# Kernel optimization log

Hardware: AMD Instinct MI355X
Metric: run time of the kernel (lower is better)

## Reference

```python
import jax, jax.numpy as jnp
import numpy as np

DIM = 64  # matches init kwarg `dim`; temperature = sqrt(DIM)


def setup_inputs() -> dict:
    key = jax.random.key(0)
    kq, kk, kv = jax.random.split(key, 3)
    B, Lq, Lk, d = 16, 4096, 4096, DIM
    q = jax.random.normal(kq, (B, Lq, d), dtype=jnp.float32)
    k = jax.random.normal(kk, (B, Lk, d), dtype=jnp.float32)
    v = jax.random.normal(kv, (B, Lk, d), dtype=jnp.float32)
    return {"q": q, "k": k, "v": v}


def reference(q, k, v):
    # attn = softmax(q @ k^T / sqrt(dim)); dropout is identity in eval mode.
    temperature = jnp.asarray(np.sqrt(DIM), dtype=q.dtype)
    scores = jnp.einsum('bqd,bkd->bqk', q, k) / temperature  # [B, Lq, Lk]
    attn = jax.nn.softmax(scores, axis=-1)
    out = jnp.einsum('bqk,bkd->bqd', attn, v)  # [B, Lq, d]
    return out
```

## Files before the change

kernel.cpp:

```cpp
#include <hip/hip_runtime.h>
#include <stdint.h>
#include <math.h>

typedef __attribute__((ext_vector_type(2)))  float f2;
typedef __attribute__((ext_vector_type(4)))  float f4;
typedef __attribute__((ext_vector_type(16))) float f32x16;
typedef __attribute__((ext_vector_type(8)))  short bf16x8;

#define NB   16
#define LSEQ 4096
#define DH   64
#define QB   128
#define KVB  64
#define NT   (LSEQ / KVB)

__device__ __forceinline__ short f2bf(float f) {
    union { float f; uint32_t u; } v; v.f = f;
    return (short)((v.u + 0x7FFFu + ((v.u >> 16) & 1u)) >> 16);
}

__device__ __forceinline__ uint32_t cvtpk(float lo, float hi) {
    uint32_t r;
    asm("v_cvt_pk_bf16_f32 %0, %1, %2" : "=v"(r) : "v"(lo), "v"(hi));
    return r;
}

__global__ __launch_bounds__(256, 2) void fa_fwd(
    const float* __restrict__ Q, const float* __restrict__ K,
    const float* __restrict__ V, float* __restrict__ O)
{
    __shared__ __align__(16) short k_lds[2][KVB * DH];
    __shared__ __align__(16) short v_lds[2][DH * KVB];

    const int tid  = threadIdx.x;
    const int lane = tid & 63;
    const int w    = tid >> 6;
    const int l31  = lane & 31;
    const int H    = lane >> 5;

    const int bid  = blockIdx.x;
    const int xcd  = bid & 7;
    const int slot = bid >> 3;
    const int b    = xcd * 2 + (slot >> 5);
    const int qt   = slot & 31;
    const int q0   = qt * QB + w * 32;

    const float* Qb = Q + (size_t)b * LSEQ * DH;
    const float* Kb = K + (size_t)b * LSEQ * DH;
    const float* Vb = V + (size_t)b * LSEQ * DH;
    float*       Ob = O + (size_t)b * LSEQ * DH;

    const float QS = 0.125f * 1.44269504088896340736f;

    bf16x8 qf[4];
#pragma unroll
    for (int kb = 0; kb < 4; ++kb) {
        const float* src = Qb + (size_t)(q0 + l31) * DH + 16 * kb + 8 * H;
        f4 a = *(const f4*)src;
        f4 c = *(const f4*)(src + 4);
        bf16x8 f;
        f[0] = f2bf(a[0] * QS); f[1] = f2bf(a[1] * QS);
        f[2] = f2bf(a[2] * QS); f[3] = f2bf(a[3] * QS);
        f[4] = f2bf(c[0] * QS); f[5] = f2bf(c[1] * QS);
        f[6] = f2bf(c[2] * QS); f[7] = f2bf(c[3] * QS);
        qf[kb] = f;
    }

    bf16x8 ones;
#pragma unroll
    for (int i = 0; i < 8; ++i) ones[i] = (short)0x3F80;

    f4 kreg[4];
    f2 vreg[8];

    const int k_kv0 = (tid >> 3);
    const int k_d0  = (tid & 7) * 8;
    const int v_d0  = (tid & 31) * 2;
    const int v_g   = tid >> 5;

#define LOADK(KV0)                                                              \
    {                                                                           \
        _Pragma("unroll")                                                       \
        for (int p = 0; p < 2; ++p) {                                           \
            const float* src = Kb + (size_t)((KV0) + k_kv0 + 32 * p) * DH + k_d0; \
            kreg[2 * p]     = *(const f4*)src;                                  \
            kreg[2 * p + 1] = *(const f4*)(src + 4);                            \
        }                                                                       \
        _Pragma("unroll")                                                       \
        for (int j = 0; j < 8; ++j)                                             \
            vreg[j] = *(const f2*)&Vb[(size_t)((KV0) + 8 * v_g + j) * DH + v_d0]; \
    }

#define WRITEK(BUF)                                                             \
    {                                                                           \
        _Pragma("unroll")                                                       \
        for (int p = 0; p < 2; ++p) {                                           \
            const int kv = k_kv0 + 32 * p;                                      \
            union { bf16x8 v; uint32_t u[4]; } t;                               \
            t.u[0] = cvtpk(kreg[2 * p][0], kreg[2 * p][1]);                     \
            t.u[1] = cvtpk(kreg[2 * p][2], kreg[2 * p][3]);                     \
            t.u[2] = cvtpk(kreg[2 * p + 1][0], kreg[2 * p + 1][1]);             \
            t.u[3] = cvtpk(kreg[2 * p + 1][2], kreg[2 * p + 1][3]);             \
            *(bf16x8*)&k_lds[BUF][kv * DH + (k_d0 ^ ((kv & 7) << 3))] = t.v;    \
        }                                                                       \
        _Pragma("unroll")                                                       \
        for (int c = 0; c < 2; ++c) {                                           \
            const int d = v_d0 + c;                                             \
            union { bf16x8 v; uint32_t u[4]; } t;                               \
            t.u[0] = cvtpk(vreg[0][c], vreg[1][c]);                             \
            t.u[1] = cvtpk(vreg[2][c], vreg[3][c]);                             \
            t.u[2] = cvtpk(vreg[4][c], vreg[5][c]);                             \
            t.u[3] = cvtpk(vreg[6][c], vreg[7][c]);                             \
            *(bf16x8*)&v_lds[BUF][d * KVB + 8 * (v_g ^ (d & 7))] = t.v;         \
        }                                                                       \
    }

#define QKH(BUF, D, ROFF)                                                       \
    {                                                                           \
        _Pragma("unroll")                                                       \
        for (int i = 0; i < 16; ++i) D[i] = 0.f;                                \
        _Pragma("unroll")                                                       \
        for (int kb = 0; kb < 4; ++kb) {                                        \
            const int d0 = 16 * kb + 8 * H;                                     \
            bf16x8 kf = *(const bf16x8*)&k_lds[BUF][(ROFF + l31) * DH + (d0 ^ ((l31 & 7) << 3))]; \
            D = __builtin_amdgcn_mfma_f32_32x32x16_bf16(kf, qf[kb], D, 0, 0, 0); \
        }                                                                       \
    }

#define EXP16(S)                                                                \
    {                                                                           \
        _Pragma("unroll")                                                       \
        for (int i = 0; i < 16; ++i) S[i] = __builtin_amdgcn_exp2f(S[i]);       \
    }

#define MAKE_PA(P, ks2, dst)                                                    \
    {                                                                           \
        uint32_t a1 = cvtpk(P[8*(ks2)+0], P[8*(ks2)+1]);                        \
        uint32_t b1 = cvtpk(P[8*(ks2)+4], P[8*(ks2)+5]);                        \
        uint32_t a2 = cvtpk(P[8*(ks2)+2], P[8*(ks2)+3]);                        \
        uint32_t b2 = cvtpk(P[8*(ks2)+6], P[8*(ks2)+7]);                        \
        asm volatile("v_permlane32_swap_b32 %0, %1" : "+v"(a1), "+v"(b1));      \
        asm volatile("v_permlane32_swap_b32 %0, %1" : "+v"(a2), "+v"(b2));      \
        union { bf16x8 v; uint32_t u[4]; } t;                                   \
        t.u[0] = a1; t.u[1] = a2; t.u[2] = b1; t.u[3] = b2;                     \
        dst = t.v;                                                              \
    }

#define PVKS(BUF, ks, pav)                                                      \
    {                                                                           \
        const int d0g = 2 * (ks) + H;                                           \
        bf16x8 vf0 = *(const bf16x8*)&v_lds[BUF][(l31)      * KVB + 8 * (d0g ^ (l31 & 7))]; \
        bf16x8 vf1 = *(const bf16x8*)&v_lds[BUF][(32 + l31) * KVB + 8 * (d0g ^ (l31 & 7))]; \
        oacc0 = __builtin_amdgcn_mfma_f32_32x32x16_bf16(vf0, pav, oacc0, 0, 0, 0); \
        oacc1 = __builtin_amdgcn_mfma_f32_32x32x16_bf16(vf1, pav, oacc1, 0, 0, 0); \
        lacc  = __builtin_amdgcn_mfma_f32_32x32x16_bf16(ones, pav, lacc, 0, 0, 0); \
    }

#define BODY(IT, DO_LOAD, DO_STAGE)                                             \
    {                                                                           \
        const int cur = (IT) & 1;                                               \
        bf16x8 pa0, pa1, pa2, pa3;                                              \
        EXP16(s0);                                                              \
        MAKE_PA(s0, 0, pa0); MAKE_PA(s0, 1, pa1);                               \
        __builtin_amdgcn_s_setprio(1);                                          \
        PVKS(cur, 0, pa0); PVKS(cur, 1, pa1);                                   \
        __builtin_amdgcn_s_setprio(0);                                          \
        EXP16(s1);                                                              \
        MAKE_PA(s1, 0, pa2); MAKE_PA(s1, 1, pa3);                               \
        __builtin_amdgcn_s_setprio(1);                                          \
        PVKS(cur, 2, pa2); PVKS(cur, 3, pa3);                                   \
        __builtin_amdgcn_s_setprio(0);                                          \
        if (DO_STAGE) {                                                         \
            WRITEK(cur ^ 1);                                                    \
            __syncthreads();                                                    \
            if (DO_LOAD) LOADK(((IT) + 2) * KVB);                               \
            __builtin_amdgcn_s_setprio(1);                                      \
            QKH(cur ^ 1, s0, 0); QKH(cur ^ 1, s1, 32);                          \
            __builtin_amdgcn_s_setprio(0);                                      \
        }                                                                       \
    }

    f32x16 oacc0, oacc1, lacc;
#pragma unroll
    for (int i = 0; i < 16; ++i) { oacc0[i] = 0.f; oacc1[i] = 0.f; lacc[i] = 0.f; }

    LOADK(0);
    WRITEK(0);
    __syncthreads();
    LOADK(KVB);

    f32x16 s0, s1;
    QKH(0, s0, 0);
    QKH(0, s1, 32);

    for (int it = 0; it < NT - 2; ++it) BODY(it, 1, 1);
    BODY(NT - 2, 0, 1);
    BODY(NT - 1, 0, 0);

    const float inv = 1.0f / lacc[0];
    const int q = q0 + l31;
#pragma unroll
    for (int k = 0; k < 4; ++k) {
        f4 o0, o1;
#pragma unroll
        for (int m = 0; m < 4; ++m) { o0[m] = oacc0[4*k+m] * inv; o1[m] = oacc1[4*k+m] * inv; }
        *(f4*)&Ob[(size_t)q * DH +      8 * k + 4 * H] = o0;
        *(f4*)&Ob[(size_t)q * DH + 32 + 8 * k + 4 * H] = o1;
    }
#undef LOADK
#undef WRITEK
#undef QKH
#undef EXP16
#undef MAKE_PA
#undef PVKS
#undef BODY
}

extern "C" void kernel_launch(void* const* d_in, const int* in_sizes, int n_in,
                              void* d_out, int out_size, void* d_ws, size_t ws_size,
                              hipStream_t stream) {
    (void)in_sizes; (void)n_in; (void)d_ws; (void)ws_size; (void)out_size;
    const float* q = (const float*)d_in[0];
    const float* k = (const float*)d_in[1];
    const float* v = (const float*)d_in[2];
    float* o = (float*)d_out;
    hipLaunchKernelGGL(fa_fwd, dim3(NB * 32), dim3(256), 0, stream, q, k, v, o);
}
```

Measured before the change: 104.7 us.

## Split KV sequence across two blocks and combine partial outputs in workspace

Templates the attention kernel on a KV split factor. With enough workspace, each (batch, query-tile) is processed by two blocks that each cover half the keys. Each block writes unnormalized partial outputs and row sums to workspace, and a second kernel adds the two halves and normalizes. This doubles the grid and raises launch bounds to four blocks per SM to improve occupancy and latency hiding. In exchange it adds a large workspace write and read-back, a second launch, and possible register pressure from the tighter launch bound.

```diff
diff --git a/kernel.cpp b/kernel.cpp
--- a/kernel.cpp
+++ b/kernel.cpp
@@ -25,12 +25,16 @@
     return r;
 }
 
-__global__ __launch_bounds__(256, 2) void fa_fwd(
+template<int NSPLIT>
+__global__ __launch_bounds__(256, 4) void fa_fwd(
     const float* __restrict__ Q, const float* __restrict__ K,
-    const float* __restrict__ V, float* __restrict__ O)
+    const float* __restrict__ V, float* __restrict__ O,
+    float* __restrict__ wsO, float* __restrict__ wsL)
 {
     __shared__ __align__(16) short k_lds[2][KVB * DH];
     __shared__ __align__(16) short v_lds[2][DH * KVB];
+
+    const int NTL = NT / NSPLIT;
 
     const int tid  = threadIdx.x;
     const int lane = tid & 63;
@@ -41,9 +45,19 @@
     const int bid  = blockIdx.x;
     const int xcd  = bid & 7;
     const int slot = bid >> 3;
-    const int b    = xcd * 2 + (slot >> 5);
-    const int qt   = slot & 31;
-    const int q0   = qt * QB + w * 32;
+    int b, h, qt;
+    if (NSPLIT == 2) {
+        const int u = slot >> 5;
+        qt = slot & 31;
+        b  = (xcd << 1) | (u >> 1);
+        h  = u & 1;
+    } else {
+        qt = slot & 31;
+        b  = xcd * 2 + (slot >> 5);
+        h  = 0;
+    }
+    const int q0     = qt * QB + w * 32;
+    const int kvbase = h * (LSEQ / NSPLIT);
 
     const float* Qb = Q + (size_t)b * LSEQ * DH;
     const float* Kb = K + (size_t)b * LSEQ * DH;
@@ -173,7 +187,7 @@
         if (DO_STAGE) {                                                         \
             WRITEK(cur ^ 1);                                                    \
             __syncthreads();                                                    \
-            if (DO_LOAD) LOADK(((IT) + 2) * KVB);                               \
+            if (DO_LOAD) LOADK(kvbase + ((IT) + 2) * KVB);                      \
             __builtin_amdgcn_s_setprio(1);                                      \
             QKH(cur ^ 1, s0, 0); QKH(cur ^ 1, s1, 32);                          \
             __builtin_amdgcn_s_setprio(0);                                      \
@@ -184,28 +198,41 @@
 #pragma unroll
     for (int i = 0; i < 16; ++i) { oacc0[i] = 0.f; oacc1[i] = 0.f; lacc[i] = 0.f; }
 
-    LOADK(0);
+    LOADK(kvbase);
     WRITEK(0);
     __syncthreads();
-    LOADK(KVB);
+    LOADK(kvbase + KVB);
 
     f32x16 s0, s1;
     QKH(0, s0, 0);
     QKH(0, s1, 32);
 
-    for (int it = 0; it < NT - 2; ++it) BODY(it, 1, 1);
-    BODY(NT - 2, 0, 1);
-    BODY(NT - 1, 0, 0);
-
-    const float inv = 1.0f / lacc[0];
+    for (int it = 0; it < NTL - 2; ++it) BODY(it, 1, 1);
+    BODY(NTL - 2, 0, 1);
+    BODY(NTL - 1, 0, 0);
+
     const int q = q0 + l31;
-#pragma unroll
-    for (int k = 0; k < 4; ++k) {
-        f4 o0, o1;
-#pragma unroll
-        for (int m = 0; m < 4; ++m) { o0[m] = oacc0[4*k+m] * inv; o1[m] = oacc1[4*k+m] * inv; }
-        *(f4*)&Ob[(size_t)q * DH +      8 * k + 4 * H] = o0;
-        *(f4*)&Ob[(size_t)q * DH + 32 + 8 * k + 4 * H] = o1;
+    if (NSPLIT == 1) {
+        const float inv = 1.0f / lacc[0];
+#pragma unroll
+        for (int k = 0; k < 4; ++k) {
+            f4 o0, o1;
+#pragma unroll
+            for (int m = 0; m < 4; ++m) { o0[m] = oacc0[4*k+m] * inv; o1[m] = oacc1[4*k+m] * inv; }
+            *(f4*)&Ob[(size_t)q * DH +      8 * k + 4 * H] = o0;
+            *(f4*)&Ob[(size_t)q * DH + 32 + 8 * k + 4 * H] = o1;
+        }
+    } else {
+        float* dst = wsO + (size_t)(h * NB + b) * LSEQ * DH;
+#pragma unroll
+        for (int k = 0; k < 4; ++k) {
+            f4 o0, o1;
+#pragma unroll
+            for (int m = 0; m < 4; ++m) { o0[m] = oacc0[4*k+m]; o1[m] = oacc1[4*k+m]; }
+            *(f4*)&dst[(size_t)q * DH +      8 * k + 4 * H] = o0;
+            *(f4*)&dst[(size_t)q * DH + 32 + 8 * k + 4 * H] = o1;
+        }
+        if (H == 0) wsL[(size_t)(h * NB + b) * LSEQ + q] = lacc[0];
     }
 #undef LOADK
 #undef WRITEK
@@ -216,13 +243,41 @@
 #undef BODY
 }
 
+__global__ __launch_bounds__(256) void fa_combine(
+    const float* __restrict__ wsO, const float* __restrict__ wsL,
+    float* __restrict__ O)
+{
+    const size_t HALF = (size_t)NB * LSEQ * DH;
+    const int idx = blockIdx.x * 256 + threadIdx.x;
+    const int row = idx >> 4;
+    f4 a = *(const f4*)&wsO[(size_t)idx * 4];
+    f4 c = *(const f4*)&wsO[HALF + (size_t)idx * 4];
+    const float inv = 1.0f / (wsL[row] + wsL[NB * LSEQ + row]);
+    f4 o;
+#pragma unroll
+    for (int m = 0; m < 4; ++m) o[m] = (a[m] + c[m]) * inv;
+    *(f4*)&O[(size_t)idx * 4] = o;
+}
+
 extern "C" void kernel_launch(void* const* d_in, const int* in_sizes, int n_in,
                               void* d_out, int out_size, void* d_ws, size_t ws_size,
                               hipStream_t stream) {
-    (void)in_sizes; (void)n_in; (void)d_ws; (void)ws_size; (void)out_size;
+    (void)in_sizes; (void)n_in; (void)out_size;
     const float* q = (const float*)d_in[0];
     const float* k = (const float*)d_in[1];
     const float* v = (const float*)d_in[2];
     float* o = (float*)d_out;
-    hipLaunchKernelGGL(fa_fwd, dim3(NB * 32), dim3(256), 0, stream, q, k, v, o);
-}
+
+    const size_t NEED = ((size_t)2 * NB * LSEQ * DH + 2 * NB * LSEQ) * sizeof(float);
+    if (ws_size >= NEED && d_ws != nullptr) {
+        float* wsO = (float*)d_ws;
+        float* wsL = wsO + (size_t)2 * NB * LSEQ * DH;
+        hipLaunchKernelGGL((fa_fwd<2>), dim3(NB * 32 * 2), dim3(256), 0, stream,
+                           q, k, v, o, wsO, wsL);
+        hipLaunchKernelGGL(fa_combine, dim3((NB * LSEQ * DH / 4) / 256), dim3(256), 0, stream,
+                           wsO, wsL, o);
+    } else {
+        hipLaunchKernelGGL((fa_fwd<1>), dim3(NB * 32), dim3(256), 0, stream,
+                           q, k, v, o, nullptr, nullptr);
+    }
+}
```

Result: slower. 279.2 us (+166.6%).

## Double query tile per block and compute row sums on VALU instead of MFMA

Applied to the files above, without the earlier changes.

Grows the query tile to 256 rows with 512 threads per block, so each staged K/V tile is reused by twice as many queries, halving global K/V loads and conversions per query. Replaces the ones-vector MFMA row-sum with a VALU accumulation of the exponentials plus a final lane shuffle, removing a third of the PV-phase MFMAs. The cost is fewer, larger blocks with wider barriers and more register pressure under the new launch bounds.

```diff
diff --git a/kernel.cpp b/kernel.cpp
--- a/kernel.cpp
+++ b/kernel.cpp
@@ -2,7 +2,6 @@
 #include <stdint.h>
 #include <math.h>
 
-typedef __attribute__((ext_vector_type(2)))  float f2;
 typedef __attribute__((ext_vector_type(4)))  float f4;
 typedef __attribute__((ext_vector_type(16))) float f32x16;
 typedef __attribute__((ext_vector_type(8)))  short bf16x8;
@@ -10,7 +9,7 @@
 #define NB   16
 #define LSEQ 4096
 #define DH   64
-#define QB   128
+#define QB   256
 #define KVB  64
 #define NT   (LSEQ / KVB)
 
@@ -25,7 +24,7 @@
     return r;
 }
 
-__global__ __launch_bounds__(256, 2) void fa_fwd(
+__global__ __launch_bounds__(512, 2) void fa_fwd(
     const float* __restrict__ Q, const float* __restrict__ K,
     const float* __restrict__ V, float* __restrict__ O)
 {
@@ -41,8 +40,8 @@
     const int bid  = blockIdx.x;
     const int xcd  = bid & 7;
     const int slot = bid >> 3;
-    const int b    = xcd * 2 + (slot >> 5);
-    const int qt   = slot & 31;
+    const int b    = xcd * 2 + (slot >> 4);
+    const int qt   = slot & 15;
     const int q0   = qt * QB + w * 32;
 
     const float* Qb = Q + (size_t)b * LSEQ * DH;
@@ -66,53 +65,38 @@
         qf[kb] = f;
     }
 
-    bf16x8 ones;
-#pragma unroll
-    for (int i = 0; i < 8; ++i) ones[i] = (short)0x3F80;
-
-    f4 kreg[4];
-    f2 vreg[8];
-
-    const int k_kv0 = (tid >> 3);
-    const int k_d0  = (tid & 7) * 8;
-    const int v_d0  = (tid & 31) * 2;
-    const int v_g   = tid >> 5;
-
-#define LOADK(KV0)                                                              \
-    {                                                                           \
-        _Pragma("unroll")                                                       \
-        for (int p = 0; p < 2; ++p) {                                           \
-            const float* src = Kb + (size_t)((KV0) + k_kv0 + 32 * p) * DH + k_d0; \
-            kreg[2 * p]     = *(const f4*)src;                                  \
-            kreg[2 * p + 1] = *(const f4*)(src + 4);                            \
-        }                                                                       \
+    f4    kreg[2];
+    float vreg[8];
+    const int k_r  = tid >> 3;
+    const int k_d0 = (tid & 7) * 8;
+    const int v_d  = tid & 63;
+    const int v_g  = tid >> 6;
+
+#define LOADT(T)                                                                \
+    {                                                                           \
+        const int kv0 = (T) * KVB;                                              \
+        const float* src = Kb + (size_t)(kv0 + k_r) * DH + k_d0;                \
+        kreg[0] = *(const f4*)src;                                              \
+        kreg[1] = *(const f4*)(src + 4);                                        \
         _Pragma("unroll")                                                       \
         for (int j = 0; j < 8; ++j)                                             \
-            vreg[j] = *(const f2*)&Vb[(size_t)((KV0) + 8 * v_g + j) * DH + v_d0]; \
-    }
-
-#define WRITEK(BUF)                                                             \
-    {                                                                           \
-        _Pragma("unroll")                                                       \
-        for (int p = 0; p < 2; ++p) {                                           \
-            const int kv = k_kv0 + 32 * p;                                      \
-            union { bf16x8 v; uint32_t u[4]; } t;                               \
-            t.u[0] = cvtpk(kreg[2 * p][0], kreg[2 * p][1]);                     \
-            t.u[1] = cvtpk(kreg[2 * p][2], kreg[2 * p][3]);                     \
-            t.u[2] = cvtpk(kreg[2 * p + 1][0], kreg[2 * p + 1][1]);             \
-            t.u[3] = cvtpk(kreg[2 * p + 1][2], kreg[2 * p + 1][3]);             \
-            *(bf16x8*)&k_lds[BUF][kv * DH + (k_d0 ^ ((kv & 7) << 3))] = t.v;    \
-        }                                                                       \
-        _Pragma("unroll")                                                       \
-        for (int c = 0; c < 2; ++c) {                                           \
-            const int d = v_d0 + c;                                             \
-            union { bf16x8 v; uint32_t u[4]; } t;                               \
-            t.u[0] = cvtpk(vreg[0][c], vreg[1][c]);                             \
-            t.u[1] = cvtpk(vreg[2][c], vreg[3][c]);                             \
-            t.u[2] = cvtpk(vreg[4][c], vreg[5][c]);                             \
-            t.u[3] = cvtpk(vreg[6][c], vreg[7][c]);                             \
-            *(bf16x8*)&v_lds[BUF][d * KVB + 8 * (v_g ^ (d & 7))] = t.v;         \
-        }                                                                       \
+            vreg[j] = Vb[(size_t)(kv0 + 8 * v_g + j) * DH + v_d];               \
+    }
+
+#define WRITET(BUF)                                                             \
+    {                                                                           \
+        union { bf16x8 v; uint32_t u[4]; } tk;                                  \
+        tk.u[0] = cvtpk(kreg[0][0], kreg[0][1]);                                \
+        tk.u[1] = cvtpk(kreg[0][2], kreg[0][3]);                                \
+        tk.u[2] = cvtpk(kreg[1][0], kreg[1][1]);                                \
+        tk.u[3] = cvtpk(kreg[1][2], kreg[1][3]);                                \
+        *(bf16x8*)&k_lds[BUF][k_r * DH + (k_d0 ^ ((k_r & 7) << 3))] = tk.v;     \
+        union { bf16x8 v; uint32_t u[4]; } tv;                                  \
+        tv.u[0] = cvtpk(vreg[0], vreg[1]);                                      \
+        tv.u[1] = cvtpk(vreg[2], vreg[3]);                                      \
+        tv.u[2] = cvtpk(vreg[4], vreg[5]);                                      \
+        tv.u[3] = cvtpk(vreg[6], vreg[7]);                                      \
+        *(bf16x8*)&v_lds[BUF][v_d * KVB + 8 * (v_g ^ (v_d & 7))] = tv.v;        \
     }
 
 #define QKH(BUF, D, ROFF)                                                       \
@@ -127,10 +111,17 @@
         }                                                                       \
     }
 
-#define EXP16(S)                                                                \
-    {                                                                           \
-        _Pragma("unroll")                                                       \
-        for (int i = 0; i < 16; ++i) S[i] = __builtin_amdgcn_exp2f(S[i]);       \
+#define EXPSUM(S)                                                               \
+    {                                                                           \
+        float r0 = 0.f, r1 = 0.f, r2 = 0.f, r3 = 0.f;                           \
+        _Pragma("unroll")                                                       \
+        for (int i = 0; i < 4; ++i) {                                           \
+            S[i]      = __builtin_amdgcn_exp2f(S[i]);      r0 += S[i];          \
+            S[i + 4]  = __builtin_amdgcn_exp2f(S[i + 4]);  r1 += S[i + 4];      \
+            S[i + 8]  = __builtin_amdgcn_exp2f(S[i + 8]);  r2 += S[i + 8];      \
+            S[i + 12] = __builtin_amdgcn_exp2f(S[i + 12]); r3 += S[i + 12];     \
+        }                                                                       \
+        l_run += (r0 + r1) + (r2 + r3);                                         \
     }
 
 #define MAKE_PA(P, ks2, dst)                                                    \
@@ -153,41 +144,41 @@
         bf16x8 vf1 = *(const bf16x8*)&v_lds[BUF][(32 + l31) * KVB + 8 * (d0g ^ (l31 & 7))]; \
         oacc0 = __builtin_amdgcn_mfma_f32_32x32x16_bf16(vf0, pav, oacc0, 0, 0, 0); \
         oacc1 = __builtin_amdgcn_mfma_f32_32x32x16_bf16(vf1, pav, oacc1, 0, 0, 0); \
-        lacc  = __builtin_amdgcn_mfma_f32_32x32x16_bf16(ones, pav, lacc, 0, 0, 0); \
     }
 
 #define BODY(IT, DO_LOAD, DO_STAGE)                                             \
     {                                                                           \
         const int cur = (IT) & 1;                                               \
         bf16x8 pa0, pa1, pa2, pa3;                                              \
-        EXP16(s0);                                                              \
+        EXPSUM(s0);                                                             \
         MAKE_PA(s0, 0, pa0); MAKE_PA(s0, 1, pa1);                               \
         __builtin_amdgcn_s_setprio(1);                                          \
         PVKS(cur, 0, pa0); PVKS(cur, 1, pa1);                                   \
         __builtin_amdgcn_s_setprio(0);                                          \
-        EXP16(s1);                                                              \
+        EXPSUM(s1);                                                             \
         MAKE_PA(s1, 0, pa2); MAKE_PA(s1, 1, pa3);                               \
         __builtin_amdgcn_s_setprio(1);                                          \
         PVKS(cur, 2, pa2); PVKS(cur, 3, pa3);                                   \
         __builtin_amdgcn_s_setprio(0);                                          \
         if (DO_STAGE) {                                                         \
-            WRITEK(cur ^ 1);                                                    \
+            WRITET(cur ^ 1);                                                    \
             __syncthreads();                                                    \
-            if (DO_LOAD) LOADK(((IT) + 2) * KVB);                               \
+            if (DO_LOAD) LOADT((IT) + 2);                                       \
             __builtin_amdgcn_s_setprio(1);                                      \
             QKH(cur ^ 1, s0, 0); QKH(cur ^ 1, s1, 32);                          \
             __builtin_amdgcn_s_setprio(0);                                      \
         }                                                                       \
     }
 
-    f32x16 oacc0, oacc1, lacc;
-#pragma unroll
-    for (int i = 0; i < 16; ++i) { oacc0[i] = 0.f; oacc1[i] = 0.f; lacc[i] = 0.f; }
-
-    LOADK(0);
-    WRITEK(0);
+    f32x16 oacc0, oacc1;
+#pragma unroll
+    for (int i = 0; i < 16; ++i) { oacc0[i] = 0.f; oacc1[i] = 0.f; }
+    float l_run = 0.f;
+
+    LOADT(0);
+    WRITET(0);
     __syncthreads();
-    LOADK(KVB);
+    LOADT(1);
 
     f32x16 s0, s1;
     QKH(0, s0, 0);
@@ -197,7 +188,8 @@
     BODY(NT - 2, 0, 1);
     BODY(NT - 1, 0, 0);
 
-    const float inv = 1.0f / lacc[0];
+    l_run += __shfl_xor(l_run, 32);
+    const float inv = 1.0f / l_run;
     const int q = q0 + l31;
 #pragma unroll
     for (int k = 0; k < 4; ++k) {
@@ -207,10 +199,10 @@
         *(f4*)&Ob[(size_t)q * DH +      8 * k + 4 * H] = o0;
         *(f4*)&Ob[(size_t)q * DH + 32 + 8 * k + 4 * H] = o1;
     }
-#undef LOADK
-#undef WRITEK
+#undef LOADT
+#undef WRITET
 #undef QKH
-#undef EXP16
+#undef EXPSUM
 #undef MAKE_PA
 #undef PVKS
 #undef BODY
@@ -224,5 +216,5 @@
     const float* k = (const float*)d_in[1];
     const float* v = (const float*)d_in[2];
     float* o = (float*)d_out;
-    hipLaunchKernelGGL(fa_fwd, dim3(NB * 32), dim3(256), 0, stream, q, k, v, o);
-}
+    hipLaunchKernelGGL(fa_fwd, dim3(NB * (LSEQ / QB)), dim3(512), 0, stream, q, k, v, o);
+}
```

Measured after the change: 87.98 us. 1.19x faster.

## Double per-wave query rows and compute softmax denominator with VALU sums

Applied to the files above, without the earlier changes.

Each wave now handles 64 query rows (two 32-row groups) instead of 32, so the Q tile per block doubles and every K/V fragment read from LDS feeds twice as many MFMAs. The grid halves to 256 blocks and launch bounds drop to one block per SIMD group, which leaves room for the extra accumulator registers. The ones-vector MFMA that computed the row sum is replaced by per-lane exp sums plus a final cross-half shuffle. In exchange the grid is smaller than two waves per CU slot, so occupancy and latency hiding may drop, and register pressure rises.

```diff
diff --git a/kernel.cpp b/kernel.cpp
--- a/kernel.cpp
+++ b/kernel.cpp
@@ -10,7 +10,7 @@
 #define NB   16
 #define LSEQ 4096
 #define DH   64
-#define QB   128
+#define QB   256
 #define KVB  64
 #define NT   (LSEQ / KVB)
 
@@ -25,7 +25,7 @@
     return r;
 }
 
-__global__ __launch_bounds__(256, 2) void fa_fwd(
+__global__ __launch_bounds__(256, 1) void fa_fwd(
     const float* __restrict__ Q, const float* __restrict__ K,
     const float* __restrict__ V, float* __restrict__ O)
 {
@@ -41,9 +41,9 @@
     const int bid  = blockIdx.x;
     const int xcd  = bid & 7;
     const int slot = bid >> 3;
-    const int b    = xcd * 2 + (slot >> 5);
-    const int qt   = slot & 31;
-    const int q0   = qt * QB + w * 32;
+    const int b    = xcd * 2 + (slot >> 4);
+    const int qt   = slot & 15;
+    const int q0   = qt * QB + w * 64;
 
     const float* Qb = Q + (size_t)b * LSEQ * DH;
     const float* Kb = K + (size_t)b * LSEQ * DH;
@@ -52,46 +52,45 @@
 
     const float QS = 0.125f * 1.44269504088896340736f;
 
-    bf16x8 qf[4];
+    bf16x8 qfA[4], qfB[4];
 #pragma unroll
     for (int kb = 0; kb < 4; ++kb) {
-        const float* src = Qb + (size_t)(q0 + l31) * DH + 16 * kb + 8 * H;
-        f4 a = *(const f4*)src;
-        f4 c = *(const f4*)(src + 4);
-        bf16x8 f;
-        f[0] = f2bf(a[0] * QS); f[1] = f2bf(a[1] * QS);
-        f[2] = f2bf(a[2] * QS); f[3] = f2bf(a[3] * QS);
-        f[4] = f2bf(c[0] * QS); f[5] = f2bf(c[1] * QS);
-        f[6] = f2bf(c[2] * QS); f[7] = f2bf(c[3] * QS);
-        qf[kb] = f;
-    }
-
-    bf16x8 ones;
-#pragma unroll
-    for (int i = 0; i < 8; ++i) ones[i] = (short)0x3F80;
+#pragma unroll
+        for (int g = 0; g < 2; ++g) {
+            const float* src = Qb + (size_t)(q0 + 32 * g + l31) * DH + 16 * kb + 8 * H;
+            f4 a = *(const f4*)src;
+            f4 c = *(const f4*)(src + 4);
+            bf16x8 f;
+            f[0] = f2bf(a[0] * QS); f[1] = f2bf(a[1] * QS);
+            f[2] = f2bf(a[2] * QS); f[3] = f2bf(a[3] * QS);
+            f[4] = f2bf(c[0] * QS); f[5] = f2bf(c[1] * QS);
+            f[6] = f2bf(c[2] * QS); f[7] = f2bf(c[3] * QS);
+            if (g == 0) qfA[kb] = f; else qfB[kb] = f;
+        }
+    }
 
     f4 kreg[4];
     f2 vreg[8];
-
     const int k_kv0 = (tid >> 3);
     const int k_d0  = (tid & 7) * 8;
     const int v_d0  = (tid & 31) * 2;
     const int v_g   = tid >> 5;
 
-#define LOADK(KV0)                                                              \
-    {                                                                           \
+#define LOADT(T)                                                                \
+    {                                                                           \
+        const int kv0 = (T) * KVB;                                              \
         _Pragma("unroll")                                                       \
         for (int p = 0; p < 2; ++p) {                                           \
-            const float* src = Kb + (size_t)((KV0) + k_kv0 + 32 * p) * DH + k_d0; \
+            const float* src = Kb + (size_t)(kv0 + k_kv0 + 32 * p) * DH + k_d0; \
             kreg[2 * p]     = *(const f4*)src;                                  \
             kreg[2 * p + 1] = *(const f4*)(src + 4);                            \
         }                                                                       \
         _Pragma("unroll")                                                       \
         for (int j = 0; j < 8; ++j)                                             \
-            vreg[j] = *(const f2*)&Vb[(size_t)((KV0) + 8 * v_g + j) * DH + v_d0]; \
-    }
-
-#define WRITEK(BUF)                                                             \
+            vreg[j] = *(const f2*)&Vb[(size_t)(kv0 + 8 * v_g + j) * DH + v_d0]; \
+    }
+
+#define WRITET(BUF)                                                             \
     {                                                                           \
         _Pragma("unroll")                                                       \
         for (int p = 0; p < 2; ++p) {                                           \
@@ -115,22 +114,33 @@
         }                                                                       \
     }
 
-#define QKH(BUF, D, ROFF)                                                       \
-    {                                                                           \
-        _Pragma("unroll")                                                       \
-        for (int i = 0; i < 16; ++i) D[i] = 0.f;                                \
+#define QK2(BUF)                                                                \
+    {                                                                           \
+        _Pragma("unroll")                                                       \
+        for (int i = 0; i < 16; ++i) { sA0[i] = 0.f; sA1[i] = 0.f; sB0[i] = 0.f; sB1[i] = 0.f; } \
         _Pragma("unroll")                                                       \
         for (int kb = 0; kb < 4; ++kb) {                                        \
             const int d0 = 16 * kb + 8 * H;                                     \
-            bf16x8 kf = *(const bf16x8*)&k_lds[BUF][(ROFF + l31) * DH + (d0 ^ ((l31 & 7) << 3))]; \
-            D = __builtin_amdgcn_mfma_f32_32x32x16_bf16(kf, qf[kb], D, 0, 0, 0); \
-        }                                                                       \
-    }
-
-#define EXP16(S)                                                                \
-    {                                                                           \
-        _Pragma("unroll")                                                       \
-        for (int i = 0; i < 16; ++i) S[i] = __builtin_amdgcn_exp2f(S[i]);       \
+            bf16x8 kf0 = *(const bf16x8*)&k_lds[BUF][(l31)      * DH + (d0 ^ ((l31 & 7) << 3))]; \
+            bf16x8 kf1 = *(const bf16x8*)&k_lds[BUF][(32 + l31) * DH + (d0 ^ ((l31 & 7) << 3))]; \
+            sA0 = __builtin_amdgcn_mfma_f32_32x32x16_bf16(kf0, qfA[kb], sA0, 0, 0, 0); \
+            sB0 = __builtin_amdgcn_mfma_f32_32x32x16_bf16(kf0, qfB[kb], sB0, 0, 0, 0); \
+            sA1 = __builtin_amdgcn_mfma_f32_32x32x16_bf16(kf1, qfA[kb], sA1, 0, 0, 0); \
+            sB1 = __builtin_amdgcn_mfma_f32_32x32x16_bf16(kf1, qfB[kb], sB1, 0, 0, 0); \
+        }                                                                       \
+    }
+
+#define EXPSUM(S, L)                                                            \
+    {                                                                           \
+        float r0 = 0.f, r1 = 0.f, r2 = 0.f, r3 = 0.f;                           \
+        _Pragma("unroll")                                                       \
+        for (int i = 0; i < 4; ++i) {                                           \
+            S[i]      = __builtin_amdgcn_exp2f(S[i]);      r0 += S[i];          \
+            S[i + 4]  = __builtin_amdgcn_exp2f(S[i + 4]);  r1 += S[i + 4];      \
+            S[i + 8]  = __builtin_amdgcn_exp2f(S[i + 8]);  r2 += S[i + 8];      \
+            S[i + 12] = __builtin_amdgcn_exp2f(S[i + 12]); r3 += S[i + 12];     \
+        }                                                                       \
+        L += (r0 + r1) + (r2 + r3);                                             \
     }
 
 #define MAKE_PA(P, ks2, dst)                                                    \
@@ -146,73 +156,83 @@
         dst = t.v;                                                              \
     }
 
-#define PVKS(BUF, ks, pav)                                                      \
+#define PVKS2(BUF, ks, pA, pB)                                                  \
     {                                                                           \
         const int d0g = 2 * (ks) + H;                                           \
         bf16x8 vf0 = *(const bf16x8*)&v_lds[BUF][(l31)      * KVB + 8 * (d0g ^ (l31 & 7))]; \
         bf16x8 vf1 = *(const bf16x8*)&v_lds[BUF][(32 + l31) * KVB + 8 * (d0g ^ (l31 & 7))]; \
-        oacc0 = __builtin_amdgcn_mfma_f32_32x32x16_bf16(vf0, pav, oacc0, 0, 0, 0); \
-        oacc1 = __builtin_amdgcn_mfma_f32_32x32x16_bf16(vf1, pav, oacc1, 0, 0, 0); \
-        lacc  = __builtin_amdgcn_mfma_f32_32x32x16_bf16(ones, pav, lacc, 0, 0, 0); \
+        oA0 = __builtin_amdgcn_mfma_f32_32x32x16_bf16(vf0, pA, oA0, 0, 0, 0);   \
+        oB0 = __builtin_amdgcn_mfma_f32_32x32x16_bf16(vf0, pB, oB0, 0, 0, 0);   \
+        oA1 = __builtin_amdgcn_mfma_f32_32x32x16_bf16(vf1, pA, oA1, 0, 0, 0);   \
+        oB1 = __builtin_amdgcn_mfma_f32_32x32x16_bf16(vf1, pB, oB1, 0, 0, 0);   \
     }
 
 #define BODY(IT, DO_LOAD, DO_STAGE)                                             \
     {                                                                           \
         const int cur = (IT) & 1;                                               \
-        bf16x8 pa0, pa1, pa2, pa3;                                              \
-        EXP16(s0);                                                              \
-        MAKE_PA(s0, 0, pa0); MAKE_PA(s0, 1, pa1);                               \
+        bf16x8 pa0, pa1, pb0, pb1;                                              \
+        EXPSUM(sA0, lA); MAKE_PA(sA0, 0, pa0); MAKE_PA(sA0, 1, pa1);            \
+        EXPSUM(sB0, lB); MAKE_PA(sB0, 0, pb0); MAKE_PA(sB0, 1, pb1);            \
         __builtin_amdgcn_s_setprio(1);                                          \
-        PVKS(cur, 0, pa0); PVKS(cur, 1, pa1);                                   \
+        PVKS2(cur, 0, pa0, pb0); PVKS2(cur, 1, pa1, pb1);                       \
         __builtin_amdgcn_s_setprio(0);                                          \
-        EXP16(s1);                                                              \
-        MAKE_PA(s1, 0, pa2); MAKE_PA(s1, 1, pa3);                               \
+        EXPSUM(sA1, lA); MAKE_PA(sA1, 0, pa0); MAKE_PA(sA1, 1, pa1);            \
+        EXPSUM(sB1, lB); MAKE_PA(sB1, 0, pb0); MAKE_PA(sB1, 1, pb1);            \
         __builtin_amdgcn_s_setprio(1);                                          \
-        PVKS(cur, 2, pa2); PVKS(cur, 3, pa3);                                   \
+        PVKS2(cur, 2, pa0, pb0); PVKS2(cur, 3, pa1, pb1);                       \
         __builtin_amdgcn_s_setprio(0);                                          \
         if (DO_STAGE) {                                                         \
-            WRITEK(cur ^ 1);                                                    \
+            WRITET(cur ^ 1);                                                    \
             __syncthreads();                                                    \
-            if (DO_LOAD) LOADK(((IT) + 2) * KVB);                               \
+            if (DO_LOAD) LOADT((IT) + 2);                                       \
             __builtin_amdgcn_s_setprio(1);                                      \
-            QKH(cur ^ 1, s0, 0); QKH(cur ^ 1, s1, 32);                          \
+            QK2(cur ^ 1);                                                       \
             __builtin_amdgcn_s_setprio(0);                                      \
         }                                                                       \
     }
 
-    f32x16 oacc0, oacc1, lacc;
-#pragma unroll
-    for (int i = 0; i < 16; ++i) { oacc0[i] = 0.f; oacc1[i] = 0.f; lacc[i] = 0.f; }
-
-    LOADK(0);
-    WRITEK(0);
+    f32x16 oA0, oA1, oB0, oB1;
+#pragma unroll
+    for (int i = 0; i < 16; ++i) { oA0[i] = 0.f; oA1[i] = 0.f; oB0[i] = 0.f; oB1[i] = 0.f; }
+    float lA = 0.f, lB = 0.f;
+
+    LOADT(0);
+    WRITET(0);
     __syncthreads();
-    LOADK(KVB);
-
-    f32x16 s0, s1;
-    QKH(0, s0, 0);
-    QKH(0, s1, 32);
+    LOADT(1);
+
+    f32x16 sA0, sA1, sB0, sB1;
+    QK2(0);
 
     for (int it = 0; it < NT - 2; ++it) BODY(it, 1, 1);
     BODY(NT - 2, 0, 1);
     BODY(NT - 1, 0, 0);
 
-    const float inv = 1.0f / lacc[0];
-    const int q = q0 + l31;
+    lA += __shfl_xor(lA, 32);
+    lB += __shfl_xor(lB, 32);
+    const float invA = 1.0f / lA;
+    const float invB = 1.0f / lB;
+    const int qA = q0 + l31;
+    const int qB = q0 + 32 + l31;
 #pragma unroll
     for (int k = 0; k < 4; ++k) {
-        f4 o0, o1;
-#pragma unroll
-        for (int m = 0; m < 4; ++m) { o0[m] = oacc0[4*k+m] * inv; o1[m] = oacc1[4*k+m] * inv; }
-        *(f4*)&Ob[(size_t)q * DH +      8 * k + 4 * H] = o0;
-        *(f4*)&Ob[(size_t)q * DH + 32 + 8 * k + 4 * H] = o1;
-    }
-#undef LOADK
-#undef WRITEK
-#undef QKH
-#undef EXP16
+        f4 a0, a1, b0, b1;
+#pragma unroll
+        for (int m = 0; m < 4; ++m) {
+            a0[m] = oA0[4*k+m] * invA; a1[m] = oA1[4*k+m] * invA;
+            b0[m] = oB0[4*k+m] * invB; b1[m] = oB1[4*k+m] * invB;
+        }
+        *(f4*)&Ob[(size_t)qA * DH +      8 * k + 4 * H] = a0;
+        *(f4*)&Ob[(size_t)qA * DH + 32 + 8 * k + 4 * H] = a1;
+        *(f4*)&Ob[(size_t)qB * DH +      8 * k + 4 * H] = b0;
+        *(f4*)&Ob[(size_t)qB * DH + 32 + 8 * k + 4 * H] = b1;
+    }
+#undef LOADT
+#undef WRITET
+#undef QK2
+#undef EXPSUM
 #undef MAKE_PA
-#undef PVKS
+#undef PVKS2
 #undef BODY
 }
 
@@ -224,5 +244,5 @@
     const float* k = (const float*)d_in[1];
     const float* v = (const float*)d_in[2];
     float* o = (float*)d_out;
-    hipLaunchKernelGGL(fa_fwd, dim3(NB * 32), dim3(256), 0, stream, q, k, v, o);
-}
+    hipLaunchKernelGGL(fa_fwd, dim3(NB * (LSEQ / QB)), dim3(256), 0, stream, q, k, v, o);
+}
```

Measured after the change: 105.7 us. About the same (+1.0%).
